# Kernel optimization log

Measured on AMD Instinct MI355X. Metric: run time of the kernel, lower is better.

Reference implementation:

```python
import jax, jax.numpy as jnp
import numpy as np

B, T, I, H, O, P = 32, 8192, 16, 128, 3, 1024


def setup_inputs() -> dict:
    key = jax.random.key(0)
    ks = jax.random.split(key, 8)
    x = jax.random.normal(ks[0], (B, T, I), dtype=jnp.float32)
    # feature channel 2 holds the photo id (original code does x[:,:,2].long())
    ids = jax.random.randint(ks[1], (B, T), 0, P)
    x = x.at[:, :, 2].set(ids.astype(jnp.float32))
    s = 1.0 / np.sqrt(H).astype(np.float32)
    W_ih = jax.random.uniform(ks[2], (4 * H, I), minval=-s, maxval=s, dtype=jnp.float32)
    W_hh = jax.random.uniform(ks[3], (4 * H, H), minval=-s, maxval=s, dtype=jnp.float32)
    b_ih = jax.random.uniform(ks[4], (4 * H,), minval=-s, maxval=s, dtype=jnp.float32)
    b_hh = jax.random.uniform(ks[5], (4 * H,), minval=-s, maxval=s, dtype=jnp.float32)
    W_fc = jax.random.uniform(ks[6], (O, H), minval=-s, maxval=s, dtype=jnp.float32)
    b_fc = jax.random.uniform(ks[7], (O,), minval=-s, maxval=s, dtype=jnp.float32)
    return dict(x=x, W_ih=W_ih, W_hh=W_hh, b_ih=b_ih, b_hh=b_hh,
                W_fc=W_fc, b_fc=b_fc, num_photos=P)


def _lstm(x, W_ih, W_hh, b_ih, b_hh):
    # single-layer batch_first LSTM, PyTorch gate order (i, f, g, o), zero init state
    Bz = x.shape[0]
    Hh = W_hh.shape[1]
    # precompute input contribution for all timesteps: [B, T, 4H]
    xg = jnp.einsum('bti,gi->btg', x, W_ih) + b_ih + b_hh

    def step(carry, gx):
        h, c = carry
        g = gx + h @ W_hh.T
        i, f, gg, o = jnp.split(g, 4, axis=-1)
        i = jax.nn.sigmoid(i)
        f = jax.nn.sigmoid(f)
        gg = jnp.tanh(gg)
        o = jax.nn.sigmoid(o)
        c = f * c + i * gg
        h = o * jnp.tanh(c)
        return (h, c), h

    h0 = jnp.zeros((Bz, Hh), x.dtype)
    _, hs = jax.lax.scan(step, (h0, h0), jnp.swapaxes(xg, 0, 1))  # [T, B, H]
    return jnp.swapaxes(hs, 0, 1)  # [B, T, H]


def reference(x, W_ih, W_hh, b_ih, b_hh, W_fc, b_fc, num_photos):
    Bz, T, _ = x.shape
    h = _lstm(x, W_ih, W_hh, b_ih, b_hh)          # [B, T, H]
    out = h @ W_fc.T + b_fc                        # [B, T, 3]
    ids = x[:, :, 2].astype(jnp.int32)             # [B, T]
    valid = ids < num_photos
    safe = jnp.where(valid, ids, 0)
    # flatten (batch, photo_id) into a single segment id per element
    seg = (jnp.arange(Bz, dtype=jnp.int32)[:, None] * num_photos + safe).reshape(-1)
    w = valid.astype(out.dtype)
    sums = jax.ops.segment_sum((out * w[..., None]).reshape(-1, out.shape[-1]),
                               seg, num_segments=Bz * num_photos)
    sums = sums.reshape(Bz, num_photos, out.shape[-1])
    counts = jax.ops.segment_sum(w.reshape(-1), seg, num_segments=Bz * num_photos)
    counts = counts.reshape(Bz, num_photos, 1)
    counts = jnp.where(counts == 0, 1.0, counts)   # matches photo_counts[photo_counts==0]=1
    return sums / counts
```

## Files before the change

### kernel.cpp

```cpp
#include <hip/hip_runtime.h>

#define B_ 32
#define T_ 8192
#define I_ 16
#define H_ 128
#define P_ 1024
#define O_ 3

typedef _Float16 h2 __attribute__((ext_vector_type(2)));
typedef _Float16 h4 __attribute__((ext_vector_type(4)));
typedef _Float16 h8 __attribute__((ext_vector_type(8)));

#if __has_builtin(__builtin_amdgcn_fdot2)
#define FDOT2(a, b, c) __builtin_amdgcn_fdot2((a), (b), (c), false)
#else
__device__ __forceinline__ float fdot2_asm(h2 a, h2 b, float c) {
    asm("v_dot2_f32_f16 %0, %1, %2, %0" : "+v"(c) : "v"(a), "v"(b));
    return c;
}
#define FDOT2(a, b, c) fdot2_asm((a), (b), (c))
#endif

#define FORME(M, g) M(g,0,0) M(g,0,1) M(g,0,2) M(g,0,3) \
                    M(g,1,0) M(g,1,1) M(g,1,2) M(g,1,3) \
                    M(g,2,0) M(g,2,1) M(g,2,2) M(g,2,3) \
                    M(g,3,0) M(g,3,1) M(g,3,2) M(g,3,3)
#define FORALL(M) FORME(M,0) FORME(M,1) FORME(M,2) FORME(M,3)
#define FORG(M) M(0) M(1) M(2) M(3)

#define DPPF(v, ctrl) \
    __int_as_float(__builtin_amdgcn_mov_dpp(__float_as_int(v), (ctrl), 0xF, 0xF, true))

__device__ __forceinline__ float xor32_add(float p) {
    float a = p, b = p;
    asm("v_permlane32_swap_b32 %0, %1" : "+v"(a), "+v"(b));
    return a + b;
}

__device__ __forceinline__ float tanh_f(float x) {
    return 2.f / (1.f + __expf(-2.f * x)) - 1.f;
}
__device__ __forceinline__ h4 cvt4(float4 v) {
    return (h4){(_Float16)v.x, (_Float16)v.y, (_Float16)v.z, (_Float16)v.w};
}

__device__ __forceinline__ void lds_barrier() {
    asm volatile("s_waitcnt lgkmcnt(0)\n\ts_barrier" ::: "memory");
}

__global__ __launch_bounds__(512, 2) __attribute__((amdgpu_waves_per_eu(2, 2)))
void lstm_fused(
    const float* __restrict__ x,
    const float* __restrict__ W_ih,
    const float* __restrict__ W_hh,
    const float* __restrict__ b_ih,
    const float* __restrict__ b_hh,
    const float* __restrict__ W_fc,
    float* __restrict__ sums,
    float* __restrict__ counts)
{
    const int b   = blockIdx.x;
    const int tid = threadIdx.x;
    const int j   = tid >> 2;
    const int kc  = tid & 3;

    __shared__ __align__(16) _Float16 hh[2][H_];
    __shared__ __align__(16) _Float16 xt[2][16 * I_];
    __shared__ float sums_lds[P_ * O_];
    __shared__ float counts_lds[P_];

    const float* wr0 = W_hh + (0 * H_ + j) * H_;
    const float* wr1 = W_hh + (1 * H_ + j) * H_;
    const float* wr2 = W_hh + (2 * H_ + j) * H_;
    const float* wr3 = W_hh + (3 * H_ + j) * H_;
    #define WLOAD(g, m, e) h2 W##g##_##m##_##e = (h2){ \
        (_Float16)wr##g[kc * 8 + 32 * (m) + 2 * (e)], \
        (_Float16)wr##g[kc * 8 + 32 * (m) + 2 * (e) + 1]};
    FORALL(WLOAD)

    #define ULOAD(g) \
        h2 U##g##_0 = (h2){(_Float16)W_ih[((g) * H_ + j) * I_ + kc * 4 + 0], \
                           (_Float16)W_ih[((g) * H_ + j) * I_ + kc * 4 + 1]}; \
        h2 U##g##_1 = (h2){(_Float16)W_ih[((g) * H_ + j) * I_ + kc * 4 + 2], \
                           (_Float16)W_ih[((g) * H_ + j) * I_ + kc * 4 + 3]};
    FORG(ULOAD)

    const float bias = b_ih[kc * H_ + j] + b_hh[kc * H_ + j];
    const float wfc  = (kc < 3) ? W_fc[kc * H_ + j] : 0.f;

    const bool fc_lane = ((tid & 0x2C) == 0) && (kc < 3);

    for (int i = tid; i < P_ * O_; i += 512) sums_lds[i] = 0.f;
    for (int i = tid; i < P_;      i += 512) counts_lds[i] = 0.f;
    if (tid < H_) hh[0][tid] = (_Float16)0.f;

    const float* xb = x + (size_t)b * T_ * I_;
    float4 xr4 = make_float4(0.f, 0.f, 0.f, 0.f);
    if (tid < 64) {
        xr4 = ((const float4*)xb)[tid];
        *(h4*)&xt[0][tid * 4] = cvt4(xr4);
    }
    float c = 0.f;
    float pend_p = 0.f;
    int   pend_id = 0;
    __syncthreads();

    #pragma unroll 1
    for (int t = 0; t < T_; ++t) {
        const int off = t & 15;
        const int btx = (t >> 4) & 1;
        const int bh  = t & 1;

        if (t != 0) {
            if (fc_lane && (unsigned)pend_id < (unsigned)P_)
                atomicAdd(&sums_lds[pend_id * O_ + kc], pend_p);
            if (tid == 0 && (unsigned)pend_id < (unsigned)P_)
                atomicAdd(&counts_lds[pend_id], 1.f);
        }

        if (tid < 64) {
            if (off == 0 && t + 16 < T_)
                xr4 = ((const float4*)(xb + (t + 16) * I_))[tid];
            if (off == 8 && t + 8 < T_)
                *(h4*)&xt[btx ^ 1][tid * 4] = cvt4(xr4);
        }

        const h4 xv4 = *(const h4*)&xt[btx][off * I_ + kc * 4];
        const h2 xv0 = __builtin_shufflevector(xv4, xv4, 0, 1);
        const h2 xv1 = __builtin_shufflevector(xv4, xv4, 2, 3);
        const int id = (int)(float)xt[btx][off * I_ + 2];

        float acc0 = 0.f, acc1 = 0.f, acc2 = 0.f, acc3 = 0.f;
        #define HD(m) { \
            h8 hv = *(const h8*)&hh[bh][kc * 8 + 32 * (m)]; \
            h2 p0 = __builtin_shufflevector(hv, hv, 0, 1); \
            h2 p1 = __builtin_shufflevector(hv, hv, 2, 3); \
            h2 p2 = __builtin_shufflevector(hv, hv, 4, 5); \
            h2 p3 = __builtin_shufflevector(hv, hv, 6, 7); \
            acc0 = FDOT2(p0, W0_##m##_0, acc0); acc0 = FDOT2(p1, W0_##m##_1, acc0); \
            acc0 = FDOT2(p2, W0_##m##_2, acc0); acc0 = FDOT2(p3, W0_##m##_3, acc0); \
            acc1 = FDOT2(p0, W1_##m##_0, acc1); acc1 = FDOT2(p1, W1_##m##_1, acc1); \
            acc1 = FDOT2(p2, W1_##m##_2, acc1); acc1 = FDOT2(p3, W1_##m##_3, acc1); \
            acc2 = FDOT2(p0, W2_##m##_0, acc2); acc2 = FDOT2(p1, W2_##m##_1, acc2); \
            acc2 = FDOT2(p2, W2_##m##_2, acc2); acc2 = FDOT2(p3, W2_##m##_3, acc2); \
            acc3 = FDOT2(p0, W3_##m##_0, acc3); acc3 = FDOT2(p1, W3_##m##_1, acc3); \
            acc3 = FDOT2(p2, W3_##m##_2, acc3); acc3 = FDOT2(p3, W3_##m##_3, acc3); }
        HD(0) HD(1) HD(2) HD(3)
        acc0 = FDOT2(xv0, U0_0, acc0); acc0 = FDOT2(xv1, U0_1, acc0);
        acc1 = FDOT2(xv0, U1_0, acc1); acc1 = FDOT2(xv1, U1_1, acc1);
        acc2 = FDOT2(xv0, U2_0, acc2); acc2 = FDOT2(xv1, U2_1, acc2);
        acc3 = FDOT2(xv0, U3_0, acc3); acc3 = FDOT2(xv1, U3_1, acc3);

        float s_;
        s_ = DPPF(acc0, 0xB1); acc0 += s_;
        s_ = DPPF(acc1, 0xB1); acc1 += s_;
        s_ = DPPF(acc2, 0xB1); acc2 += s_;
        s_ = DPPF(acc3, 0xB1); acc3 += s_;
        s_ = DPPF(acc0, 0x4E); acc0 += s_;
        s_ = DPPF(acc1, 0x4E); acc1 += s_;
        s_ = DPPF(acc2, 0x4E); acc2 += s_;
        s_ = DPPF(acc3, 0x4E); acc3 += s_;

        float tg = (kc == 0) ? acc0 : (kc == 1) ? acc1 : (kc == 2) ? acc2 : acc3;
        tg += bias;
        const bool  isg = (kc == 2);
        const float arg = isg ? (tg + tg) : tg;
        const float sf  = 1.f / (1.f + __expf(-arg));
        const float act = isg ? (sf + sf - 1.f) : sf;

        const float gi = DPPF(act, 0x00);
        const float gf = DPPF(act, 0x55);
        const float gg = DPPF(act, 0xAA);
        const float go = DPPF(act, 0xFF);
        c = fmaf(gf, c, gi * gg);
        const float hnew = go * tanh_f(c);

        if (kc == 0) hh[bh ^ 1][j] = (_Float16)hnew;

        float p = hnew * wfc;
        p += DPPF(p, 0x124);
        p += DPPF(p, 0x128);
        p = xor32_add(p);
        pend_p  = p;
        pend_id = id;

        lds_barrier();
    }

    if (fc_lane && (unsigned)pend_id < (unsigned)P_)
        atomicAdd(&sums_lds[pend_id * O_ + kc], pend_p);
    if (tid == 0 && (unsigned)pend_id < (unsigned)P_)
        atomicAdd(&counts_lds[pend_id], 1.f);
    __syncthreads();

    float* sums_g = sums + (size_t)b * P_ * O_;
    for (int i = tid; i < P_ * O_; i += 512) sums_g[i] = sums_lds[i];
    float* cnt_g = counts + (size_t)b * P_;
    for (int i = tid; i < P_; i += 512) cnt_g[i] = counts_lds[i];
}

__global__ void finalize_kernel(const float* __restrict__ sums,
                                const float* __restrict__ counts,
                                const float* __restrict__ b_fc,
                                float* __restrict__ out)
{
    const int idx = blockIdx.x * blockDim.x + threadIdx.x;
    if (idx >= B_ * P_ * O_) return;
    const int o  = idx % O_;
    const int bp = idx / O_;
    const float cnt = counts[bp];
    const float denom = (cnt > 0.f) ? cnt : 1.f;
    out[idx] = (sums[idx] + cnt * b_fc[o]) / denom;
}

extern "C" void kernel_launch(void* const* d_in, const int* in_sizes, int n_in,
                              void* d_out, int out_size, void* d_ws, size_t ws_size,
                              hipStream_t stream) {
    const float* x    = (const float*)d_in[0];
    const float* W_ih = (const float*)d_in[1];
    const float* W_hh = (const float*)d_in[2];
    const float* b_ih = (const float*)d_in[3];
    const float* b_hh = (const float*)d_in[4];
    const float* W_fc = (const float*)d_in[5];
    const float* b_fc = (const float*)d_in[6];

    float* out    = (float*)d_out;
    float* sums   = (float*)d_ws;
    float* counts = sums + (size_t)B_ * P_ * O_;

    lstm_fused<<<B_, 512, 0, stream>>>(x, W_ih, W_hh, b_ih, b_hh, W_fc, sums, counts);

    const int n = B_ * P_ * O_;
    finalize_kernel<<<(n + 255) / 256, 256, 0, stream>>>(sums, counts, b_fc, out);
}
```

Before: 6.112 ms.

## Halve block size so each lane computes two hidden units per step

Each block now runs 256 threads instead of 512, and each 4-lane group handles two hidden units (ja, jb) instead of one, holding twice the recurrent weights in registers. The goal is fewer waves per barrier, cheaper s_barrier sync in the serial timestep loop, and reuse of each loaded h vector across two rows. The cost is twice the FDOT2 work per lane on the critical path and higher register pressure, with a risk of spills. The fc_lane reduction mask and the x-prefetch logic (tid<64) are unchanged, and the pairwise partial p now combines both units.

Result: no change. 6.057 ms (-0.9%).

```diff
diff --git a/kernel.cpp b/kernel.cpp
--- a/kernel.cpp
+++ b/kernel.cpp
@@ -48,7 +48,7 @@
     asm volatile("s_waitcnt lgkmcnt(0)\n\ts_barrier" ::: "memory");
 }
 
-__global__ __launch_bounds__(512, 2) __attribute__((amdgpu_waves_per_eu(2, 2)))
+__global__ __launch_bounds__(256, 1) __attribute__((amdgpu_waves_per_eu(1, 1)))
 void lstm_fused(
     const float* __restrict__ x,
     const float* __restrict__ W_ih,
@@ -61,37 +61,55 @@
 {
     const int b   = blockIdx.x;
     const int tid = threadIdx.x;
-    const int j   = tid >> 2;
+    const int q   = tid >> 2;
     const int kc  = tid & 3;
+    const int ja  = 2 * q;
+    const int jb  = 2 * q + 1;
 
     __shared__ __align__(16) _Float16 hh[2][H_];
     __shared__ __align__(16) _Float16 xt[2][16 * I_];
     __shared__ float sums_lds[P_ * O_];
     __shared__ float counts_lds[P_];
 
-    const float* wr0 = W_hh + (0 * H_ + j) * H_;
-    const float* wr1 = W_hh + (1 * H_ + j) * H_;
-    const float* wr2 = W_hh + (2 * H_ + j) * H_;
-    const float* wr3 = W_hh + (3 * H_ + j) * H_;
-    #define WLOAD(g, m, e) h2 W##g##_##m##_##e = (h2){ \
-        (_Float16)wr##g[kc * 8 + 32 * (m) + 2 * (e)], \
-        (_Float16)wr##g[kc * 8 + 32 * (m) + 2 * (e) + 1]};
-    FORALL(WLOAD)
-
-    #define ULOAD(g) \
-        h2 U##g##_0 = (h2){(_Float16)W_ih[((g) * H_ + j) * I_ + kc * 4 + 0], \
-                           (_Float16)W_ih[((g) * H_ + j) * I_ + kc * 4 + 1]}; \
-        h2 U##g##_1 = (h2){(_Float16)W_ih[((g) * H_ + j) * I_ + kc * 4 + 2], \
-                           (_Float16)W_ih[((g) * H_ + j) * I_ + kc * 4 + 3]};
-    FORG(ULOAD)
-
-    const float bias = b_ih[kc * H_ + j] + b_hh[kc * H_ + j];
-    const float wfc  = (kc < 3) ? W_fc[kc * H_ + j] : 0.f;
+    const float* wrA0 = W_hh + (0 * H_ + ja) * H_;
+    const float* wrA1 = W_hh + (1 * H_ + ja) * H_;
+    const float* wrA2 = W_hh + (2 * H_ + ja) * H_;
+    const float* wrA3 = W_hh + (3 * H_ + ja) * H_;
+    const float* wrB0 = W_hh + (0 * H_ + jb) * H_;
+    const float* wrB1 = W_hh + (1 * H_ + jb) * H_;
+    const float* wrB2 = W_hh + (2 * H_ + jb) * H_;
+    const float* wrB3 = W_hh + (3 * H_ + jb) * H_;
+    #define WLOADA(g, m, e) h2 WA##g##_##m##_##e = (h2){ \
+        (_Float16)wrA##g[kc * 8 + 32 * (m) + 2 * (e)], \
+        (_Float16)wrA##g[kc * 8 + 32 * (m) + 2 * (e) + 1]};
+    #define WLOADB(g, m, e) h2 WB##g##_##m##_##e = (h2){ \
+        (_Float16)wrB##g[kc * 8 + 32 * (m) + 2 * (e)], \
+        (_Float16)wrB##g[kc * 8 + 32 * (m) + 2 * (e) + 1]};
+    FORALL(WLOADA)
+    FORALL(WLOADB)
+
+    #define ULOADA(g) \
+        h2 UA##g##_0 = (h2){(_Float16)W_ih[((g) * H_ + ja) * I_ + kc * 4 + 0], \
+                            (_Float16)W_ih[((g) * H_ + ja) * I_ + kc * 4 + 1]}; \
+        h2 UA##g##_1 = (h2){(_Float16)W_ih[((g) * H_ + ja) * I_ + kc * 4 + 2], \
+                            (_Float16)W_ih[((g) * H_ + ja) * I_ + kc * 4 + 3]};
+    #define ULOADB(g) \
+        h2 UB##g##_0 = (h2){(_Float16)W_ih[((g) * H_ + jb) * I_ + kc * 4 + 0], \
+                            (_Float16)W_ih[((g) * H_ + jb) * I_ + kc * 4 + 1]}; \
+        h2 UB##g##_1 = (h2){(_Float16)W_ih[((g) * H_ + jb) * I_ + kc * 4 + 2], \
+                            (_Float16)W_ih[((g) * H_ + jb) * I_ + kc * 4 + 3]};
+    FORG(ULOADA)
+    FORG(ULOADB)
+
+    const float biasA = b_ih[kc * H_ + ja] + b_hh[kc * H_ + ja];
+    const float biasB = b_ih[kc * H_ + jb] + b_hh[kc * H_ + jb];
+    const float wfcA  = (kc < 3) ? W_fc[kc * H_ + ja] : 0.f;
+    const float wfcB  = (kc < 3) ? W_fc[kc * H_ + jb] : 0.f;
 
     const bool fc_lane = ((tid & 0x2C) == 0) && (kc < 3);
 
-    for (int i = tid; i < P_ * O_; i += 512) sums_lds[i] = 0.f;
-    for (int i = tid; i < P_;      i += 512) counts_lds[i] = 0.f;
+    for (int i = tid; i < P_ * O_; i += 256) sums_lds[i] = 0.f;
+    for (int i = tid; i < P_;      i += 256) counts_lds[i] = 0.f;
     if (tid < H_) hh[0][tid] = (_Float16)0.f;
 
     const float* xb = x + (size_t)b * T_ * I_;
@@ -100,7 +118,7 @@
         xr4 = ((const float4*)xb)[tid];
         *(h4*)&xt[0][tid * 4] = cvt4(xr4);
     }
-    float c = 0.f;
+    float cA = 0.f, cB = 0.f;
     float pend_p = 0.f;
     int   pend_id = 0;
     __syncthreads();
@@ -130,54 +148,89 @@
         const h2 xv1 = __builtin_shufflevector(xv4, xv4, 2, 3);
         const int id = (int)(float)xt[btx][off * I_ + 2];
 
-        float acc0 = 0.f, acc1 = 0.f, acc2 = 0.f, acc3 = 0.f;
+        float aA0 = 0.f, aA1 = 0.f, aA2 = 0.f, aA3 = 0.f;
+        float aB0 = 0.f, aB1 = 0.f, aB2 = 0.f, aB3 = 0.f;
         #define HD(m) { \
             h8 hv = *(const h8*)&hh[bh][kc * 8 + 32 * (m)]; \
             h2 p0 = __builtin_shufflevector(hv, hv, 0, 1); \
             h2 p1 = __builtin_shufflevector(hv, hv, 2, 3); \
             h2 p2 = __builtin_shufflevector(hv, hv, 4, 5); \
             h2 p3 = __builtin_shufflevector(hv, hv, 6, 7); \
-            acc0 = FDOT2(p0, W0_##m##_0, acc0); acc0 = FDOT2(p1, W0_##m##_1, acc0); \
-            acc0 = FDOT2(p2, W0_##m##_2, acc0); acc0 = FDOT2(p3, W0_##m##_3, acc0); \
-            acc1 = FDOT2(p0, W1_##m##_0, acc1); acc1 = FDOT2(p1, W1_##m##_1, acc1); \
-            acc1 = FDOT2(p2, W1_##m##_2, acc1); acc1 = FDOT2(p3, W1_##m##_3, acc1); \
-            acc2 = FDOT2(p0, W2_##m##_0, acc2); acc2 = FDOT2(p1, W2_##m##_1, acc2); \
-            acc2 = FDOT2(p2, W2_##m##_2, acc2); acc2 = FDOT2(p3, W2_##m##_3, acc2); \
-            acc3 = FDOT2(p0, W3_##m##_0, acc3); acc3 = FDOT2(p1, W3_##m##_1, acc3); \
-            acc3 = FDOT2(p2, W3_##m##_2, acc3); acc3 = FDOT2(p3, W3_##m##_3, acc3); }
+            aA0 = FDOT2(p0, WA0_##m##_0, aA0); aA0 = FDOT2(p1, WA0_##m##_1, aA0); \
+            aA0 = FDOT2(p2, WA0_##m##_2, aA0); aA0 = FDOT2(p3, WA0_##m##_3, aA0); \
+            aA1 = FDOT2(p0, WA1_##m##_0, aA1); aA1 = FDOT2(p1, WA1_##m##_1, aA1); \
+            aA1 = FDOT2(p2, WA1_##m##_2, aA1); aA1 = FDOT2(p3, WA1_##m##_3, aA1); \
+            aA2 = FDOT2(p0, WA2_##m##_0, aA2); aA2 = FDOT2(p1, WA2_##m##_1, aA2); \
+            aA2 = FDOT2(p2, WA2_##m##_2, aA2); aA2 = FDOT2(p3, WA2_##m##_3, aA2); \
+            aA3 = FDOT2(p0, WA3_##m##_0, aA3); aA3 = FDOT2(p1, WA3_##m##_1, aA3); \
+            aA3 = FDOT2(p2, WA3_##m##_2, aA3); aA3 = FDOT2(p3, WA3_##m##_3, aA3); \
+            aB0 = FDOT2(p0, WB0_##m##_0, aB0); aB0 = FDOT2(p1, WB0_##m##_1, aB0); \
+            aB0 = FDOT2(p2, WB0_##m##_2, aB0); aB0 = FDOT2(p3, WB0_##m##_3, aB0); \
+            aB1 = FDOT2(p0, WB1_##m##_0, aB1); aB1 = FDOT2(p1, WB1_##m##_1, aB1); \
+            aB1 = FDOT2(p2, WB1_##m##_2, aB1); aB1 = FDOT2(p3, WB1_##m##_3, aB1); \
+            aB2 = FDOT2(p0, WB2_##m##_0, aB2); aB2 = FDOT2(p1, WB2_##m##_1, aB2); \
+            aB2 = FDOT2(p2, WB2_##m##_2, aB2); aB2 = FDOT2(p3, WB2_##m##_3, aB2); \
+            aB3 = FDOT2(p0, WB3_##m##_0, aB3); aB3 = FDOT2(p1, WB3_##m##_1, aB3); \
+            aB3 = FDOT2(p2, WB3_##m##_2, aB3); aB3 = FDOT2(p3, WB3_##m##_3, aB3); }
         HD(0) HD(1) HD(2) HD(3)
-        acc0 = FDOT2(xv0, U0_0, acc0); acc0 = FDOT2(xv1, U0_1, acc0);
-        acc1 = FDOT2(xv0, U1_0, acc1); acc1 = FDOT2(xv1, U1_1, acc1);
-        acc2 = FDOT2(xv0, U2_0, acc2); acc2 = FDOT2(xv1, U2_1, acc2);
-        acc3 = FDOT2(xv0, U3_0, acc3); acc3 = FDOT2(xv1, U3_1, acc3);
+        aA0 = FDOT2(xv0, UA0_0, aA0); aA0 = FDOT2(xv1, UA0_1, aA0);
+        aA1 = FDOT2(xv0, UA1_0, aA1); aA1 = FDOT2(xv1, UA1_1, aA1);
+        aA2 = FDOT2(xv0, UA2_0, aA2); aA2 = FDOT2(xv1, UA2_1, aA2);
+        aA3 = FDOT2(xv0, UA3_0, aA3); aA3 = FDOT2(xv1, UA3_1, aA3);
+        aB0 = FDOT2(xv0, UB0_0, aB0); aB0 = FDOT2(xv1, UB0_1, aB0);
+        aB1 = FDOT2(xv0, UB1_0, aB1); aB1 = FDOT2(xv1, UB1_1, aB1);
+        aB2 = FDOT2(xv0, UB2_0, aB2); aB2 = FDOT2(xv1, UB2_1, aB2);
+        aB3 = FDOT2(xv0, UB3_0, aB3); aB3 = FDOT2(xv1, UB3_1, aB3);
 
         float s_;
-        s_ = DPPF(acc0, 0xB1); acc0 += s_;
-        s_ = DPPF(acc1, 0xB1); acc1 += s_;
-        s_ = DPPF(acc2, 0xB1); acc2 += s_;
-        s_ = DPPF(acc3, 0xB1); acc3 += s_;
-        s_ = DPPF(acc0, 0x4E); acc0 += s_;
-        s_ = DPPF(acc1, 0x4E); acc1 += s_;
-        s_ = DPPF(acc2, 0x4E); acc2 += s_;
-        s_ = DPPF(acc3, 0x4E); acc3 += s_;
-
-        float tg = (kc == 0) ? acc0 : (kc == 1) ? acc1 : (kc == 2) ? acc2 : acc3;
-        tg += bias;
-        const bool  isg = (kc == 2);
-        const float arg = isg ? (tg + tg) : tg;
-        const float sf  = 1.f / (1.f + __expf(-arg));
-        const float act = isg ? (sf + sf - 1.f) : sf;
-
-        const float gi = DPPF(act, 0x00);
-        const float gf = DPPF(act, 0x55);
-        const float gg = DPPF(act, 0xAA);
-        const float go = DPPF(act, 0xFF);
-        c = fmaf(gf, c, gi * gg);
-        const float hnew = go * tanh_f(c);
-
-        if (kc == 0) hh[bh ^ 1][j] = (_Float16)hnew;
-
-        float p = hnew * wfc;
+        s_ = DPPF(aA0, 0xB1); aA0 += s_;
+        s_ = DPPF(aA1, 0xB1); aA1 += s_;
+        s_ = DPPF(aA2, 0xB1); aA2 += s_;
+        s_ = DPPF(aA3, 0xB1); aA3 += s_;
+        s_ = DPPF(aB0, 0xB1); aB0 += s_;
+        s_ = DPPF(aB1, 0xB1); aB1 += s_;
+        s_ = DPPF(aB2, 0xB1); aB2 += s_;
+        s_ = DPPF(aB3, 0xB1); aB3 += s_;
+        s_ = DPPF(aA0, 0x4E); aA0 += s_;
+        s_ = DPPF(aA1, 0x4E); aA1 += s_;
+        s_ = DPPF(aA2, 0x4E); aA2 += s_;
+        s_ = DPPF(aA3, 0x4E); aA3 += s_;
+        s_ = DPPF(aB0, 0x4E); aB0 += s_;
+        s_ = DPPF(aB1, 0x4E); aB1 += s_;
+        s_ = DPPF(aB2, 0x4E); aB2 += s_;
+        s_ = DPPF(aB3, 0x4E); aB3 += s_;
+
+        float tgA = (kc == 0) ? aA0 : (kc == 1) ? aA1 : (kc == 2) ? aA2 : aA3;
+        float tgB = (kc == 0) ? aB0 : (kc == 1) ? aB1 : (kc == 2) ? aB2 : aB3;
+        tgA += biasA;
+        tgB += biasB;
+        const bool  isg  = (kc == 2);
+        const float argA = isg ? (tgA + tgA) : tgA;
+        const float argB = isg ? (tgB + tgB) : tgB;
+        const float sfA  = 1.f / (1.f + __expf(-argA));
+        const float sfB  = 1.f / (1.f + __expf(-argB));
+        const float actA = isg ? (sfA + sfA - 1.f) : sfA;
+        const float actB = isg ? (sfB + sfB - 1.f) : sfB;
+
+        const float giA = DPPF(actA, 0x00);
+        const float gfA = DPPF(actA, 0x55);
+        const float ggA = DPPF(actA, 0xAA);
+        const float goA = DPPF(actA, 0xFF);
+        const float giB = DPPF(actB, 0x00);
+        const float gfB = DPPF(actB, 0x55);
+        const float ggB = DPPF(actB, 0xAA);
+        const float goB = DPPF(actB, 0xFF);
+        cA = fmaf(gfA, cA, giA * ggA);
+        cB = fmaf(gfB, cB, giB * ggB);
+        const float hnA = goA * tanh_f(cA);
+        const float hnB = goB * tanh_f(cB);
+
+        if (kc == 0) {
+            h2 hp = (h2){(_Float16)hnA, (_Float16)hnB};
+            *(h2*)&hh[bh ^ 1][ja] = hp;
+        }
+
+        float p = fmaf(hnA, wfcA, hnB * wfcB);
         p += DPPF(p, 0x124);
         p += DPPF(p, 0x128);
         p = xor32_add(p);
@@ -194,9 +247,9 @@
     __syncthreads();
 
     float* sums_g = sums + (size_t)b * P_ * O_;
-    for (int i = tid; i < P_ * O_; i += 512) sums_g[i] = sums_lds[i];
+    for (int i = tid; i < P_ * O_; i += 256) sums_g[i] = sums_lds[i];
     float* cnt_g = counts + (size_t)b * P_;
-    for (int i = tid; i < P_; i += 512) cnt_g[i] = counts_lds[i];
+    for (int i = tid; i < P_; i += 256) cnt_g[i] = counts_lds[i];
 }
 
 __global__ void finalize_kernel(const float* __restrict__ sums,
@@ -228,7 +281,7 @@
     float* sums   = (float*)d_ws;
     float* counts = sums + (size_t)B_ * P_ * O_;
 
-    lstm_fused<<<B_, 512, 0, stream>>>(x, W_ih, W_hh, b_ih, b_hh, W_fc, sums, counts);
+    lstm_fused<<<B_, 256, 0, stream>>>(x, W_ih, W_hh, b_ih, b_hh, W_fc, sums, counts);
 
     const int n = B_ * P_ * O_;
     finalize_kernel<<<(n + 255) / 256, 256, 0, stream>>>(sums, counts, b_fc, out);
```

## Precompute input gate projections in separate kernel and stream them into recurrence

Applied to the files above, without the earlier changes.

Adds a parallel pre-pass kernel that computes x·W_ih + biases for every timestep in fp16, written gate-major to workspace, plus a u16 photo-id array. The recurrent kernel then reads one precomputed gate value per lane per step from registers, prefetched in 8-step chunks, instead of staging x in LDS and doing extra dot products on the serial critical path. This costs a large workspace buffer (~268 MB) and extra global traffic. If the workspace is too small it falls back to the original kernel.

After: 6.113 ms. About the same (+0.0%).

```diff
diff --git a/kernel.cpp b/kernel.cpp
--- a/kernel.cpp
+++ b/kernel.cpp
@@ -6,10 +6,12 @@
 #define H_ 128
 #define P_ 1024
 #define O_ 3
+#define R_ 512
 
 typedef _Float16 h2 __attribute__((ext_vector_type(2)));
 typedef _Float16 h4 __attribute__((ext_vector_type(4)));
 typedef _Float16 h8 __attribute__((ext_vector_type(8)));
+typedef unsigned short u16;
 
 #if __has_builtin(__builtin_amdgcn_fdot2)
 #define FDOT2(a, b, c) __builtin_amdgcn_fdot2((a), (b), (c), false)
@@ -43,18 +45,69 @@
 __device__ __forceinline__ h4 cvt4(float4 v) {
     return (h4){(_Float16)v.x, (_Float16)v.y, (_Float16)v.z, (_Float16)v.w};
 }
-
 __device__ __forceinline__ void lds_barrier() {
     asm volatile("s_waitcnt lgkmcnt(0)\n\ts_barrier" ::: "memory");
 }
 
-__global__ __launch_bounds__(512, 2) __attribute__((amdgpu_waves_per_eu(2, 2)))
-void lstm_fused(
+
+__global__ __launch_bounds__(256)
+void xg_precompute(
     const float* __restrict__ x,
     const float* __restrict__ W_ih,
-    const float* __restrict__ W_hh,
     const float* __restrict__ b_ih,
     const float* __restrict__ b_hh,
+    _Float16* __restrict__ xg,
+    u16* __restrict__ ids)
+{
+    const int nchunk = T_ / 64;
+    const int b   = blockIdx.x / nchunk;
+    const int t0  = (blockIdx.x % nchunk) * 64;
+    const int tid = threadIdx.x;
+
+    __shared__ __align__(16) float xs[64][I_];
+
+    ((float4*)xs)[tid] = ((const float4*)(x + ((size_t)b * T_ + t0) * I_))[tid];
+    __syncthreads();
+    if (tid < 64)
+        ids[(size_t)b * T_ + t0 + tid] = (u16)(int)xs[tid][2];
+
+    const int r0 = tid * 2;
+    float w0[I_], w1[I_];
+    #pragma unroll
+    for (int i = 0; i < I_; ++i) {
+        w0[i] = W_ih[r0 * I_ + i];
+        w1[i] = W_ih[(r0 + 1) * I_ + i];
+    }
+    const float bb0 = b_ih[r0] + b_hh[r0];
+    const float bb1 = b_ih[r0 + 1] + b_hh[r0 + 1];
+
+    _Float16* o0 = xg + ((size_t)b * R_ + r0) * T_ + t0;
+    _Float16* o1 = o0 + T_;
+    #pragma unroll 1
+    for (int cc = 0; cc < 8; ++cc) {
+        h8 v0, v1;
+        #pragma unroll
+        for (int kk = 0; kk < 8; ++kk) {
+            const float* xr = xs[cc * 8 + kk];
+            float a0 = bb0, a1 = bb1;
+            #pragma unroll
+            for (int i2 = 0; i2 < I_; ++i2) {
+                a0 = fmaf(w0[i2], xr[i2], a0);
+                a1 = fmaf(w1[i2], xr[i2], a1);
+            }
+            v0[kk] = (_Float16)a0;
+            v1[kk] = (_Float16)a1;
+        }
+        *(h8*)&o0[cc * 8] = v0;
+        *(h8*)&o1[cc * 8] = v1;
+    }
+}
+
+__global__ __launch_bounds__(512, 2) __attribute__((amdgpu_waves_per_eu(2, 2)))
+void lstm_fused_xg(
+    const _Float16* __restrict__ xg,
+    const u16* __restrict__ ids,
+    const float* __restrict__ W_hh,
     const float* __restrict__ W_fc,
     float* __restrict__ sums,
     float* __restrict__ counts)
@@ -65,7 +118,6 @@
     const int kc  = tid & 3;
 
     __shared__ __align__(16) _Float16 hh[2][H_];
-    __shared__ __align__(16) _Float16 xt[2][16 * I_];
     __shared__ float sums_lds[P_ * O_];
     __shared__ float counts_lds[P_];
 
@@ -78,6 +130,139 @@
         (_Float16)wr##g[kc * 8 + 32 * (m) + 2 * (e) + 1]};
     FORALL(WLOAD)
 
+    const float wfc = (kc < 3) ? W_fc[kc * H_ + j] : 0.f;
+    const bool fc_lane = ((tid & 0x2C) == 0) && (kc < 3);
+
+    for (int i = tid; i < P_ * O_; i += 512) sums_lds[i] = 0.f;
+    for (int i = tid; i < P_;      i += 512) counts_lds[i] = 0.f;
+    if (tid < H_) hh[0][tid] = (_Float16)0.f;
+
+    const _Float16* xgp = xg + ((size_t)b * R_ + kc * H_ + j) * T_;
+    const u16*      idp = ids + (size_t)b * T_;
+
+    h8    xc  = *(const h8*)&xgp[0];
+    h8    xn  = *(const h8*)&xgp[8];
+    uint4 idc = *(const uint4*)&idp[0];
+    uint4 idn = *(const uint4*)&idp[8];
+
+    float c = 0.f;
+    float pend_p = 0.f;
+    int   pend_id = 0;
+    __syncthreads();
+
+    #pragma unroll 1
+    for (int tt = 0; tt < T_; tt += 8) {
+        #pragma unroll
+        for (int k = 0; k < 8; ++k) {
+            const int bh = k & 1;
+
+            if (k != 0 || tt != 0) {
+                if (fc_lane && (unsigned)pend_id < (unsigned)P_)
+                    atomicAdd(&sums_lds[pend_id * O_ + kc], pend_p);
+                if (tid == 0 && (unsigned)pend_id < (unsigned)P_)
+                    atomicAdd(&counts_lds[pend_id], 1.f);
+            }
+
+            float acc0 = 0.f, acc1 = 0.f, acc2 = 0.f, acc3 = 0.f;
+            #define HD(m) { \
+                h8 hv = *(const h8*)&hh[bh][kc * 8 + 32 * (m)]; \
+                h2 p0 = __builtin_shufflevector(hv, hv, 0, 1); \
+                h2 p1 = __builtin_shufflevector(hv, hv, 2, 3); \
+                h2 p2 = __builtin_shufflevector(hv, hv, 4, 5); \
+                h2 p3 = __builtin_shufflevector(hv, hv, 6, 7); \
+                acc0 = FDOT2(p0, W0_##m##_0, acc0); acc0 = FDOT2(p1, W0_##m##_1, acc0); \
+                acc0 = FDOT2(p2, W0_##m##_2, acc0); acc0 = FDOT2(p3, W0_##m##_3, acc0); \
+                acc1 = FDOT2(p0, W1_##m##_0, acc1); acc1 = FDOT2(p1, W1_##m##_1, acc1); \
+                acc1 = FDOT2(p2, W1_##m##_2, acc1); acc1 = FDOT2(p3, W1_##m##_3, acc1); \
+                acc2 = FDOT2(p0, W2_##m##_0, acc2); acc2 = FDOT2(p1, W2_##m##_1, acc2); \
+                acc2 = FDOT2(p2, W2_##m##_2, acc2); acc2 = FDOT2(p3, W2_##m##_3, acc2); \
+                acc3 = FDOT2(p0, W3_##m##_0, acc3); acc3 = FDOT2(p1, W3_##m##_1, acc3); \
+                acc3 = FDOT2(p2, W3_##m##_2, acc3); acc3 = FDOT2(p3, W3_##m##_3, acc3); }
+            HD(0) HD(1) HD(2) HD(3)
+            #undef HD
+
+            float s_;
+            s_ = DPPF(acc0, 0xB1); acc0 += s_;
+            s_ = DPPF(acc1, 0xB1); acc1 += s_;
+            s_ = DPPF(acc2, 0xB1); acc2 += s_;
+            s_ = DPPF(acc3, 0xB1); acc3 += s_;
+            s_ = DPPF(acc0, 0x4E); acc0 += s_;
+            s_ = DPPF(acc1, 0x4E); acc1 += s_;
+            s_ = DPPF(acc2, 0x4E); acc2 += s_;
+            s_ = DPPF(acc3, 0x4E); acc3 += s_;
+
+            float tg = (kc == 0) ? acc0 : (kc == 1) ? acc1 : (kc == 2) ? acc2 : acc3;
+            tg += (float)xc[k];
+            const bool  isg = (kc == 2);
+            const float arg = isg ? (tg + tg) : tg;
+            const float sf  = 1.f / (1.f + __expf(-arg));
+            const float act = isg ? (sf + sf - 1.f) : sf;
+
+            const float gi = DPPF(act, 0x00);
+            const float gf = DPPF(act, 0x55);
+            const float gg = DPPF(act, 0xAA);
+            const float go = DPPF(act, 0xFF);
+            c = fmaf(gf, c, gi * gg);
+            const float hnew = go * tanh_f(c);
+
+            if (kc == 0) hh[bh ^ 1][j] = (_Float16)hnew;
+
+            float p = hnew * wfc;
+            p += DPPF(p, 0x124);
+            p += DPPF(p, 0x128);
+            p = xor32_add(p);
+            pend_p = p;
+            const unsigned idw = (k < 2) ? idc.x : (k < 4) ? idc.y
+                               : (k < 6) ? idc.z : idc.w;
+            pend_id = (int)((idw >> ((k & 1) * 16)) & 0xffffu);
+
+            lds_barrier();
+        }
+        xc = xn; idc = idn;
+        if (tt + 16 < T_) {
+            xn  = *(const h8*)&xgp[tt + 16];
+            idn = *(const uint4*)&idp[tt + 16];
+        }
+    }
+
+    if (fc_lane && (unsigned)pend_id < (unsigned)P_)
+        atomicAdd(&sums_lds[pend_id * O_ + kc], pend_p);
+    if (tid == 0 && (unsigned)pend_id < (unsigned)P_)
+        atomicAdd(&counts_lds[pend_id], 1.f);
+    __syncthreads();
+
+    float* sums_g = sums + (size_t)b * P_ * O_;
+    for (int i = tid; i < P_ * O_; i += 512) sums_g[i] = sums_lds[i];
+    float* cnt_g = counts + (size_t)b * P_;
+    for (int i = tid; i < P_; i += 512) cnt_g[i] = counts_lds[i];
+}
+
+__global__ __launch_bounds__(512, 2) __attribute__((amdgpu_waves_per_eu(2, 2)))
+void lstm_fused_fb(
+    const float* __restrict__ x, const float* __restrict__ W_ih,
+    const float* __restrict__ W_hh, const float* __restrict__ b_ih,
+    const float* __restrict__ b_hh, const float* __restrict__ W_fc,
+    float* __restrict__ sums, float* __restrict__ counts)
+{
+    const int b   = blockIdx.x;
+    const int tid = threadIdx.x;
+    const int j   = tid >> 2;
+    const int kc  = tid & 3;
+
+    __shared__ __align__(16) _Float16 hh[2][H_];
+    __shared__ __align__(16) _Float16 xt[2][16 * I_];
+    __shared__ float sums_lds[P_ * O_];
+    __shared__ float counts_lds[P_];
+
+    const float* wr0 = W_hh + (0 * H_ + j) * H_;
+    const float* wr1 = W_hh + (1 * H_ + j) * H_;
+    const float* wr2 = W_hh + (2 * H_ + j) * H_;
+    const float* wr3 = W_hh + (3 * H_ + j) * H_;
+    #define WLOADF(g, m, e) h2 W##g##_##m##_##e = (h2){ \
+        (_Float16)wr##g[kc * 8 + 32 * (m) + 2 * (e)], \
+        (_Float16)wr##g[kc * 8 + 32 * (m) + 2 * (e) + 1]};
+    FORALL(WLOADF)
+
     #define ULOAD(g) \
         h2 U##g##_0 = (h2){(_Float16)W_ih[((g) * H_ + j) * I_ + kc * 4 + 0], \
                            (_Float16)W_ih[((g) * H_ + j) * I_ + kc * 4 + 1]}; \
@@ -87,7 +272,6 @@
 
     const float bias = b_ih[kc * H_ + j] + b_hh[kc * H_ + j];
     const float wfc  = (kc < 3) ? W_fc[kc * H_ + j] : 0.f;
-
     const bool fc_lane = ((tid & 0x2C) == 0) && (kc < 3);
 
     for (int i = tid; i < P_ * O_; i += 512) sums_lds[i] = 0.f;
@@ -131,7 +315,7 @@
         const int id = (int)(float)xt[btx][off * I_ + 2];
 
         float acc0 = 0.f, acc1 = 0.f, acc2 = 0.f, acc3 = 0.f;
-        #define HD(m) { \
+        #define HDF(m) { \
             h8 hv = *(const h8*)&hh[bh][kc * 8 + 32 * (m)]; \
             h2 p0 = __builtin_shufflevector(hv, hv, 0, 1); \
             h2 p1 = __builtin_shufflevector(hv, hv, 2, 3); \
@@ -145,7 +329,7 @@
             acc2 = FDOT2(p2, W2_##m##_2, acc2); acc2 = FDOT2(p3, W2_##m##_3, acc2); \
             acc3 = FDOT2(p0, W3_##m##_0, acc3); acc3 = FDOT2(p1, W3_##m##_1, acc3); \
             acc3 = FDOT2(p2, W3_##m##_2, acc3); acc3 = FDOT2(p3, W3_##m##_3, acc3); }
-        HD(0) HD(1) HD(2) HD(3)
+        HDF(0) HDF(1) HDF(2) HDF(3)
         acc0 = FDOT2(xv0, U0_0, acc0); acc0 = FDOT2(xv1, U0_1, acc0);
         acc1 = FDOT2(xv0, U1_0, acc1); acc1 = FDOT2(xv1, U1_1, acc1);
         acc2 = FDOT2(xv0, U2_0, acc2); acc2 = FDOT2(xv1, U2_1, acc2);
@@ -227,8 +411,20 @@
     float* out    = (float*)d_out;
     float* sums   = (float*)d_ws;
     float* counts = sums + (size_t)B_ * P_ * O_;
-
-    lstm_fused<<<B_, 512, 0, stream>>>(x, W_ih, W_hh, b_ih, b_hh, W_fc, sums, counts);
+    const size_t ids_off = 524288;
+    const size_t xg_off  = 1048576;
+    const size_t need    = xg_off + (size_t)B_ * R_ * T_ * sizeof(_Float16);
+
+    if (ws_size >= need) {
+        u16*      ids = (u16*)((char*)d_ws + ids_off);
+        _Float16* xg  = (_Float16*)((char*)d_ws + xg_off);
+        xg_precompute<<<B_ * (T_ / 64), 256, 0, stream>>>(x, W_ih, b_ih, b_hh,
+                                                          xg, ids);
+        lstm_fused_xg<<<B_, 512, 0, stream>>>(xg, ids, W_hh, W_fc, sums, counts);
+    } else {
+        lstm_fused_fb<<<B_, 512, 0, stream>>>(x, W_ih, W_hh, b_ih, b_hh, W_fc,
+                                              sums, counts);
+    }
 
     const int n = B_ * P_ * O_;
     finalize_kernel<<<(n + 255) / 256, 256, 0, stream>>>(sums, counts, b_fc, out);
```
